# Optimization experiments

Measured on AMD Instinct MI355X. Metric: run time of the kernel, lower is better.

Reference implementation:

```python
import jax, jax.numpy as jnp
import numpy as np

HIDDEN = 4096
N_HEADS = 32
N_KV_HEADS = 8
HEAD_DIM = HIDDEN // N_HEADS  # 128
KV_DIM = N_KV_HEADS * HEAD_DIM  # 1024
ROPE_THETA = 10000.0
B, S = 1, 2048


def setup_inputs() -> dict:
    key = jax.random.key(0)
    ks = jax.random.split(key, 5)
    scale = 0.02
    return {
        "positions": jnp.arange(B * S, dtype=jnp.int32).reshape(B, S),
        "hidden_states": jax.random.normal(ks[0], (B, S, HIDDEN), dtype=jnp.float32),
        "Wqkv": jax.random.normal(ks[1], (HIDDEN, HIDDEN + 2 * KV_DIM), dtype=jnp.float32) * scale,
        "bqkv": jax.random.normal(ks[2], (HIDDEN + 2 * KV_DIM,), dtype=jnp.float32) * scale,
        "Wproj": jax.random.normal(ks[3], (HIDDEN, HIDDEN), dtype=jnp.float32) * scale,
        "bproj": jax.random.normal(ks[4], (HIDDEN,), dtype=jnp.float32) * scale,
    }


def _apply_rope(x, positions):
    # x: [B, S, H, D]; NeoX-style rotation over full head_dim (vLLM get_rope default)
    half = HEAD_DIM // 2
    inv_freq = 1.0 / (ROPE_THETA ** (jnp.arange(0, half, dtype=jnp.float32) / half))
    angles = positions.astype(jnp.float32)[..., None] * inv_freq  # [B, S, half]
    cos = jnp.cos(angles)[:, :, None, :]  # [B, S, 1, half]
    sin = jnp.sin(angles)[:, :, None, :]
    x1, x2 = x[..., :half], x[..., half:]
    return jnp.concatenate([x1 * cos - x2 * sin, x2 * cos + x1 * sin], axis=-1)


def reference(positions, hidden_states, Wqkv, bqkv, Wproj, bproj):
    b, s, _ = hidden_states.shape
    qkv = hidden_states @ Wqkv + bqkv  # [B, S, HIDDEN + 2*KV_DIM]
    q, k, v = jnp.split(qkv, [HIDDEN, HIDDEN + KV_DIM], axis=-1)
    q = q.reshape(b, s, N_HEADS, HEAD_DIM)
    k = k.reshape(b, s, N_KV_HEADS, HEAD_DIM)
    v = v.reshape(b, s, N_KV_HEADS, HEAD_DIM)

    q = _apply_rope(q, positions)
    k = _apply_rope(k, positions)

    # GQA: expand kv heads to query heads (4 query heads per kv head)
    rep = N_HEADS // N_KV_HEADS
    k = jnp.repeat(k, rep, axis=2)  # [B, S, N_HEADS, D]
    v = jnp.repeat(v, rep, axis=2)

    scaling = 1.0 / np.sqrt(HEAD_DIM).astype(np.float32)
    scores = jnp.einsum("bqhd,bkhd->bhqk", q, k) * scaling  # [B, H, S, S]
    causal = jnp.tril(jnp.ones((s, s), dtype=bool))
    scores = jnp.where(causal[None, None], scores, jnp.finfo(scores.dtype).min)
    probs = jax.nn.softmax(scores, axis=-1)
    attn = jnp.einsum("bhqk,bkhd->bqhd", probs, v).reshape(b, s, HIDDEN)

    return attn @ Wproj + bproj
```

## Files before the change

### kernel.cpp

```cpp
#include <hip/hip_runtime.h>

#define HIDDEN 4096
#define NHEADS 32
#define NKV 8
#define HD 128
#define KVD 1024
#define QKVN 6144
#define SEQ 2048

typedef unsigned short u16;
typedef __bf16 bf16x8 __attribute__((ext_vector_type(8)));
typedef float f32x4 __attribute__((ext_vector_type(4)));
typedef unsigned short u16x4 __attribute__((ext_vector_type(4)));

__device__ __forceinline__ u16 f2b(float f) {
  union { float f; unsigned u; } v; v.f = f;
  unsigned r = (v.u + 0x7fffu + ((v.u >> 16) & 1u)) >> 16;
  return (u16)r;
}

__device__ __forceinline__ float b2f(u16 b) {
  union { unsigned u; float f; } v; v.u = ((unsigned)b) << 16;
  return v.f;
}

__device__ __forceinline__ void gl_lds16(const void* g, void* l) {
  __builtin_amdgcn_global_load_lds(
      (const __attribute__((address_space(1))) unsigned*)g,
      (__attribute__((address_space(3))) unsigned*)l, 16, 0, 0);
}

__device__ __forceinline__ f32x4 mfma16(bf16x8 a, bf16x8 b, f32x4 c) {
  return __builtin_amdgcn_mfma_f32_16x16x32_bf16(a, b, c, 0, 0, 0);
}

__global__ void cvt_bf16(const float* __restrict__ x, u16* __restrict__ y, int n) {
  int i = (blockIdx.x * 256 + threadIdx.x) * 4;
  if (i < n) {
    float4 v = *(const float4*)(x + i);
    u16x4 o = {f2b(v.x), f2b(v.y), f2b(v.z), f2b(v.w)};
    *(u16x4*)(y + i) = o;
  }
}

__global__ void transpose_cvt64(const float* __restrict__ W, long ldW,
                                u16* __restrict__ Wt, long ldT) {
  __shared__ float tile[64][65];
  long c0 = blockIdx.x * 64L, r0 = blockIdx.y * 64L;
  int tx = threadIdx.x, ty = threadIdx.y;
#pragma unroll
  for (int i = 0; i < 4; ++i) {
    float4 v = *(const float4*)(W + (r0 + ty + i * 16) * ldW + c0 + tx * 4);
    tile[ty + i * 16][tx * 4 + 0] = v.x;
    tile[ty + i * 16][tx * 4 + 1] = v.y;
    tile[ty + i * 16][tx * 4 + 2] = v.z;
    tile[ty + i * 16][tx * 4 + 3] = v.w;
  }
  __syncthreads();
#pragma unroll
  for (int i = 0; i < 4; ++i) {
    int c = ty + i * 16;
    u16x4 o = {f2b(tile[tx * 4 + 0][c]), f2b(tile[tx * 4 + 1][c]),
               f2b(tile[tx * 4 + 2][c]), f2b(tile[tx * 4 + 3][c])};
    *(u16x4*)(Wt + (c0 + c) * ldT + r0 + tx * 4) = o;
  }
}

__global__ void transpose_b16(const u16* __restrict__ W, long ldW,
                              u16* __restrict__ Wt, long ldT) {
  __shared__ float tile[64][65];
  long c0 = blockIdx.x * 64L, r0 = blockIdx.y * 64L;
  int tx = threadIdx.x, ty = threadIdx.y;
#pragma unroll
  for (int i = 0; i < 4; ++i) {
    u16x4 v = *(const u16x4*)(W + (r0 + ty + i * 16) * ldW + c0 + tx * 4);
    tile[ty + i * 16][tx * 4 + 0] = b2f(v.x);
    tile[ty + i * 16][tx * 4 + 1] = b2f(v.y);
    tile[ty + i * 16][tx * 4 + 2] = b2f(v.z);
    tile[ty + i * 16][tx * 4 + 3] = b2f(v.w);
  }
  __syncthreads();
#pragma unroll
  for (int i = 0; i < 4; ++i) {
    int c = ty + i * 16;
    u16x4 o = {f2b(tile[tx * 4 + 0][c]), f2b(tile[tx * 4 + 1][c]),
               f2b(tile[tx * 4 + 2][c]), f2b(tile[tx * 4 + 3][c])};
    *(u16x4*)(Wt + (c0 + c) * ldT + r0 + tx * 4) = o;
  }
}

__global__ __launch_bounds__(256) void gemm_bt_bias(
    const u16* __restrict__ A, const u16* __restrict__ Bt,
    const float* __restrict__ bias, float* __restrict__ C,
    int M, int N, int K) {
  __shared__ u16 As[128 * 32];
  __shared__ u16 Bs[128 * 32];
  const int t = threadIdx.x;
  const int w = t >> 6, lane = t & 63, quad = lane >> 4, l15 = lane & 15;
  const int wy = w >> 1, wx = w & 1;
  const long m0 = blockIdx.y * 128L, n0 = blockIdx.x * 128L;
  f32x4 acc[4][4] = {};
  const u16* Ag = A + (m0 + (t >> 2)) * (long)K + (t & 3) * 8;
  const u16* Bg = Bt + (n0 + (t >> 2)) * (long)K + (t & 3) * 8;
  char* lA0 = (char*)As + w * 1024;
  char* lA1 = (char*)As + 4096 + w * 1024;
  char* lB0 = (char*)Bs + w * 1024;
  char* lB1 = (char*)Bs + 4096 + w * 1024;
  const long k64 = 64L * K;
  for (int k0 = 0; k0 < K; k0 += 32) {
    gl_lds16(Ag + k0, lA0);
    gl_lds16(Ag + k64 + k0, lA1);
    gl_lds16(Bg + k0, lB0);
    gl_lds16(Bg + k64 + k0, lB1);
    __syncthreads();
    bf16x8 af[4], bfr[4];
#pragma unroll
    for (int mi = 0; mi < 4; ++mi)
      af[mi] = *reinterpret_cast<const bf16x8*>(&As[(wy * 64 + mi * 16 + l15) * 32 + quad * 8]);
#pragma unroll
    for (int nj = 0; nj < 4; ++nj)
      bfr[nj] = *reinterpret_cast<const bf16x8*>(&Bs[(wx * 64 + nj * 16 + l15) * 32 + quad * 8]);
#pragma unroll
    for (int mi = 0; mi < 4; ++mi)
#pragma unroll
      for (int nj = 0; nj < 4; ++nj)
        acc[mi][nj] = mfma16(af[mi], bfr[nj], acc[mi][nj]);
    __syncthreads();
  }
#pragma unroll
  for (int mi = 0; mi < 4; ++mi) {
#pragma unroll
    for (int nj = 0; nj < 4; ++nj) {
      long n = n0 + wx * 64 + nj * 16 + l15;
      float bv = bias[n];
      long mrow = m0 + wy * 64 + mi * 16 + quad * 4;
#pragma unroll
      for (int r = 0; r < 4; ++r)
        C[(mrow + r) * (long)N + n] = acc[mi][nj][r] + bv;
    }
  }
}

__global__ __launch_bounds__(256) void gemm_bt_bias_b16(
    const u16* __restrict__ A, const u16* __restrict__ Bt,
    const float* __restrict__ bias, u16* __restrict__ C,
    int M, int N, int K) {
  __shared__ u16 As[128 * 32];
  __shared__ u16 Bs[128 * 32];
  const int t = threadIdx.x;
  const int w = t >> 6, lane = t & 63, quad = lane >> 4, l15 = lane & 15;
  const int wy = w >> 1, wx = w & 1;
  const long m0 = blockIdx.y * 128L, n0 = blockIdx.x * 128L;
  f32x4 acc[4][4] = {};
  const u16* Ag = A + (m0 + (t >> 2)) * (long)K + (t & 3) * 8;
  const u16* Bg = Bt + (n0 + (t >> 2)) * (long)K + (t & 3) * 8;
  char* lA0 = (char*)As + w * 1024;
  char* lA1 = (char*)As + 4096 + w * 1024;
  char* lB0 = (char*)Bs + w * 1024;
  char* lB1 = (char*)Bs + 4096 + w * 1024;
  const long k64 = 64L * K;
  for (int k0 = 0; k0 < K; k0 += 32) {
    gl_lds16(Ag + k0, lA0);
    gl_lds16(Ag + k64 + k0, lA1);
    gl_lds16(Bg + k0, lB0);
    gl_lds16(Bg + k64 + k0, lB1);
    __syncthreads();
    bf16x8 af[4], bfr[4];
#pragma unroll
    for (int mi = 0; mi < 4; ++mi)
      af[mi] = *reinterpret_cast<const bf16x8*>(&As[(wy * 64 + mi * 16 + l15) * 32 + quad * 8]);
#pragma unroll
    for (int nj = 0; nj < 4; ++nj)
      bfr[nj] = *reinterpret_cast<const bf16x8*>(&Bs[(wx * 64 + nj * 16 + l15) * 32 + quad * 8]);
#pragma unroll
    for (int mi = 0; mi < 4; ++mi)
#pragma unroll
      for (int nj = 0; nj < 4; ++nj)
        acc[mi][nj] = mfma16(af[mi], bfr[nj], acc[mi][nj]);
    __syncthreads();
  }
#pragma unroll
  for (int mi = 0; mi < 4; ++mi) {
#pragma unroll
    for (int nj = 0; nj < 4; ++nj) {
      long n = n0 + wx * 64 + nj * 16 + l15;
      float bv = bias[n];
      long mrow = m0 + wy * 64 + mi * 16 + quad * 4;
#pragma unroll
      for (int r = 0; r < 4; ++r)
        C[(mrow + r) * (long)N + n] = f2b(acc[mi][nj][r] + bv);
    }
  }
}

__global__ void rope_qk(const u16* __restrict__ qkv, const int* __restrict__ pos,
                        u16* __restrict__ Qr, u16* __restrict__ Kr) {
  int s = blockIdx.x;
  int hl = threadIdx.x >> 6;
  int d = threadIdx.x & 63;
  int h = blockIdx.y * 4 + hl;
  float p = (float)pos[s];
  float inv = __builtin_amdgcn_exp2f(-(float)d * (13.287712379549449f / 64.0f));
  float ang = p * inv;
  float cs, sn;
  __sincosf(ang, &sn, &cs);
  long base = (long)s * QKVN + (long)h * HD;
  float x1 = b2f(qkv[base + d]), x2 = b2f(qkv[base + d + 64]);
  float o1 = x1 * cs - x2 * sn, o2 = x2 * cs + x1 * sn;
  if (h < NHEADS) {
    const float sc = 0.12751744154f;
    long ob = ((long)h * SEQ + s) * HD;
    Qr[ob + d] = f2b(o1 * sc);
    Qr[ob + d + 64] = f2b(o2 * sc);
  } else {
    long ob = ((long)(h - NHEADS) * SEQ + s) * HD;
    Kr[ob + d] = f2b(o1);
    Kr[ob + d + 64] = f2b(o2);
  }
}

__device__ __forceinline__ void attn_tile(
    const bf16x8 q[4], const u16* KsF, const u16* VsF, u16* Psw,
    bool diag, int wq, int quad, int l15, int sq, f32x4 Oa[8], f32x4& lacc,
    bf16x8 ones) {
  f32x4 s[4] = {};
#pragma unroll
  for (int ks = 0; ks < 4; ++ks) {
#pragma unroll
    for (int nj = 0; nj < 4; ++nj) {
      bf16x8 bk = *reinterpret_cast<const bf16x8*>(
          &KsF[ks * 2048 + (nj * 16 + l15) * 32 + sq * 8]);
      s[nj] = mfma16(q[ks], bk, s[nj]);
    }
  }
#pragma unroll
  for (int nj = 0; nj < 4; ++nj) {
    int key = nj * 16 + l15;
    int ksw = key >> 5, kc = key & 31;
    int khi = kc >> 3, klo = kc & 7;
#pragma unroll
    for (int r = 0; r < 4; ++r) {
      float x = s[nj][r];
      if (diag && key > wq + r) x = -3.0e30f;
      int row = quad * 4 + r;
      Psw[ksw * 512 + row * 32 + ((khi ^ ((row >> 1) & 3)) << 3) + klo] =
          f2b(__builtin_amdgcn_exp2f(x));
    }
  }
#pragma unroll
  for (int ks = 0; ks < 2; ++ks) {
    bf16x8 ap = *reinterpret_cast<const bf16x8*>(&Psw[ks * 512 + l15 * 32 + sq * 8]);
    lacc = mfma16(ap, ones, lacc);
#pragma unroll
    for (int dj = 0; dj < 8; ++dj) {
      bf16x8 bv = *reinterpret_cast<const bf16x8*>(
          &VsF[ks * 4096 + (dj * 16 + l15) * 32 + sq * 8]);
      Oa[dj] = mfma16(ap, bv, Oa[dj]);
    }
  }
}

__global__ __launch_bounds__(256) void attn_fused(
    const u16* __restrict__ Qr, const u16* __restrict__ Kr,
    const u16* __restrict__ Vt, u16* __restrict__ Ao) {
  __shared__ u16 Ks[4 * 64 * 32];
  __shared__ u16 Vs[2 * 128 * 32];
  __shared__ u16 Ps[4][2 * 16 * 32];
  const int px = blockIdx.x, h = blockIdx.y, kvh = h >> 2;
  const int qtA = px, qtB = (SEQ / 64 - 1) - px;
  const int t = threadIdx.x, w = t >> 6, lane = t & 63;
  const int quad = lane >> 4, l15 = lane & 15;
  const int sq = quad ^ ((l15 >> 1) & 3);
  const int wq = w * 16 + quad * 4;
  u16* Psw = &Ps[w][0];

  bf16x8 ones;
  {
    union { u16 u[8]; bf16x8 v; } ou;
#pragma unroll
    for (int i = 0; i < 8; ++i) ou.u[i] = 0x3F80;
    ones = ou.v;
  }

  const long go = (long)(w * 16 + (lane >> 2)) * HD +
                  (long)(((lane & 3) ^ ((lane >> 3) & 3)) * 8);

  bf16x8 qA[4], qB[4];
  {
    const u16* QgA = Qr + ((long)h * SEQ + qtA * 64) * HD;
    const u16* QgB = Qr + ((long)h * SEQ + qtB * 64) * HD;
#pragma unroll
    for (int j = 0; j < 4; ++j) {
      gl_lds16(QgA + go + j * 32, (char*)Ks + j * 4096 + w * 1024);
      gl_lds16(QgB + go + j * 32, (char*)Vs + j * 4096 + w * 1024);
    }
    __syncthreads();
#pragma unroll
    for (int j = 0; j < 4; ++j) {
      qA[j] = *reinterpret_cast<const bf16x8*>(&Ks[j * 2048 + (w * 16 + l15) * 32 + sq * 8]);
      qB[j] = *reinterpret_cast<const bf16x8*>(&Vs[j * 2048 + (w * 16 + l15) * 32 + sq * 8]);
    }
    __syncthreads();
  }

  f32x4 OaA[8] = {}, OaB[8] = {};
  f32x4 lA = {}, lB = {};
  const u16* Kg0 = Kr + (long)kvh * SEQ * HD;
  const u16* Vg0 = Vt + (long)kvh * HD * SEQ;

  for (int kt = 0; kt <= qtB; ++kt) {
    const int k0 = kt * 64;
    {
      const u16* Kg = Kg0 + (long)k0 * HD;
#pragma unroll
      for (int j = 0; j < 4; ++j)
        gl_lds16(Kg + go + j * 32, (char*)Ks + j * 4096 + w * 1024);
      const u16* Vg = Vg0 + k0;
      const int vc = ((lane & 3) ^ ((lane >> 3) & 3)) * 8;
#pragma unroll
      for (int j = 0; j < 4; ++j) {
        int dd = (j & 1) * 64 + w * 16 + (lane >> 2);
        int ks = j >> 1;
        gl_lds16(Vg + (long)dd * SEQ + ks * 32 + vc, (char*)Vs + j * 4096 + w * 1024);
      }
    }
    __syncthreads();

    attn_tile(qB, Ks, Vs, Psw, kt == qtB, wq, quad, l15, sq, OaB, lB, ones);
    if (kt <= qtA)
      attn_tile(qA, Ks, Vs, Psw, kt == qtA, wq, quad, l15, sq, OaA, lA, ones);

    __syncthreads();
  }

#pragma unroll
  for (int r = 0; r < 4; ++r) {
    float invA = 1.0f / lA[r];
    float invB = 1.0f / lB[r];
    long rowA = (long)(qtA * 64 + w * 16 + quad * 4 + r) * HIDDEN + (long)h * HD;
    long rowB = (long)(qtB * 64 + w * 16 + quad * 4 + r) * HIDDEN + (long)h * HD;
#pragma unroll
    for (int dj = 0; dj < 8; ++dj) {
      Ao[rowA + dj * 16 + l15] = f2b(OaA[dj][r] * invA);
      Ao[rowB + dj * 16 + l15] = f2b(OaB[dj][r] * invB);
    }
  }
}

extern "C" void kernel_launch(void* const* d_in, const int* in_sizes, int n_in,
                              void* d_out, int out_size, void* d_ws, size_t ws_size,
                              hipStream_t stream) {
  const int* positions = (const int*)d_in[0];
  const float* hidden = (const float*)d_in[1];
  const float* Wqkv = (const float*)d_in[2];
  const float* bqkv = (const float*)d_in[3];
  const float* Wproj = (const float*)d_in[4];
  const float* bproj = (const float*)d_in[5];
  float* out = (float*)d_out;
  char* ws = (char*)d_ws;

  u16* Wqt = (u16*)(ws);
  u16* Wpt = (u16*)(ws + 50331648L);
  u16* Xb = (u16*)(ws + 83886080L);
  u16* QKVb = (u16*)(ws + 100663296L);
  u16* Qr = (u16*)(ws + 125829120L);
  u16* Kr = (u16*)(ws + 142606336L);
  u16* Vt = (u16*)(ws + 146800640L);
  u16* Ao = (u16*)(ws + 150994944L);

  cvt_bf16<<<8192, 256, 0, stream>>>(hidden, Xb, SEQ * HIDDEN);
  transpose_cvt64<<<dim3(QKVN / 64, HIDDEN / 64), dim3(16, 16), 0, stream>>>(Wqkv, QKVN, Wqt, HIDDEN);
  transpose_cvt64<<<dim3(HIDDEN / 64, HIDDEN / 64), dim3(16, 16), 0, stream>>>(Wproj, HIDDEN, Wpt, HIDDEN);
  gemm_bt_bias_b16<<<dim3(QKVN / 128, SEQ / 128), 256, 0, stream>>>(Xb, Wqt, bqkv, QKVb, SEQ, QKVN, HIDDEN);
  rope_qk<<<dim3(SEQ, 10), 256, 0, stream>>>(QKVb, positions, Qr, Kr);
  transpose_b16<<<dim3(KVD / 64, SEQ / 64), dim3(16, 16), 0, stream>>>(QKVb + 5120, QKVN, Vt, SEQ);
  attn_fused<<<dim3(SEQ / 128, NHEADS), 256, 0, stream>>>(Qr, Kr, Vt, Ao);
  gemm_bt_bias<<<dim3(HIDDEN / 128, SEQ / 128), 256, 0, stream>>>(Ao, Wpt, bproj, out, SEQ, HIDDEN, HIDDEN);
}
```

Before: 574.6 us.

## Replace GEMMs with 256x256 double-buffered, swizzled-LDS, pipelined MFMA kernel

```diff
diff --git a/kernel.cpp b/kernel.cpp
--- a/kernel.cpp
+++ b/kernel.cpp
@@ -34,6 +34,11 @@
   return __builtin_amdgcn_mfma_f32_16x16x32_bf16(a, b, c, 0, 0, 0);
 }
 
+#define BARRIER() __builtin_amdgcn_s_barrier()
+#define WAIT_LGKM0() asm volatile("s_waitcnt lgkmcnt(0)" ::: "memory")
+#define WAIT_VM6() asm volatile("s_waitcnt vmcnt(6)" ::: "memory")
+#define WAIT_VM0() asm volatile("s_waitcnt vmcnt(0)" ::: "memory")
+
 __global__ void cvt_bf16(const float* __restrict__ x, u16* __restrict__ y, int n) {
   int i = (blockIdx.x * 256 + threadIdx.x) * 4;
   if (i < n) {
@@ -89,106 +94,148 @@
   }
 }
 
-__global__ __launch_bounds__(256) void gemm_bt_bias(
+
+#define LOAD_AF(lA, QM)                                                   \
+  _Pragma("unroll") for (int mi_ = 0; mi_ < 4; ++mi_) {                   \
+    const int ro_ = (wm * 128 + (QM) * 64 + mi_ * 16 + l15) * 64;         \
+    af[mi_][0] = *(const bf16x8*)&(lA)[ro_ + sq0];                        \
+    af[mi_][1] = *(const bf16x8*)&(lA)[ro_ + sq1];                        \
+  }
+
+#define LOAD_BF(lB, QN, DST)                                              \
+  _Pragma("unroll") for (int nj_ = 0; nj_ < 2; ++nj_) {                   \
+    const int ro_ = (wn * 64 + (QN) * 32 + nj_ * 16 + l15) * 64;          \
+    DST[nj_][0] = *(const bf16x8*)&(lB)[ro_ + sq0];                       \
+    DST[nj_][1] = *(const bf16x8*)&(lB)[ro_ + sq1];                       \
+  }
+
+#define MFMA_BLOCK(MI0, NJ0, BFARR)                                       \
+  __builtin_amdgcn_s_setprio(1);                                          \
+  _Pragma("unroll") for (int mi_ = 0; mi_ < 4; ++mi_)                     \
+  _Pragma("unroll") for (int nj_ = 0; nj_ < 2; ++nj_)                     \
+  _Pragma("unroll") for (int ks_ = 0; ks_ < 2; ++ks_)                     \
+    acc[(MI0) + mi_][(NJ0) + nj_] =                                       \
+        mfma16(af[mi_][ks_], BFARR[nj_][ks_], acc[(MI0) + mi_][(NJ0) + nj_]); \
+  __builtin_amdgcn_s_setprio(0);
+
+#define STAGE_A(buf, u, kt)                                               \
+  { char* d_ = dA[u] + (buf) * 32768;                                     \
+    gl_lds16(aS[u][0] + (long)(kt) * 64, d_);                             \
+    gl_lds16(aS[u][1] + (long)(kt) * 64, d_ + 1024); }
+
+#define STAGE_B(buf, u, kt)                                               \
+  { char* d_ = dB[u] + (buf) * 32768;                                     \
+    gl_lds16(bS[u][0] + (long)(kt) * 64, d_);                             \
+    gl_lds16(bS[u][1] + (long)(kt) * 64, d_ + 1024); }
+
+template <bool OUT16>
+__global__ __launch_bounds__(512) void gemm256_bt_bias(
     const u16* __restrict__ A, const u16* __restrict__ Bt,
-    const float* __restrict__ bias, float* __restrict__ C,
+    const float* __restrict__ bias, void* __restrict__ Cv,
     int M, int N, int K) {
-  __shared__ u16 As[128 * 32];
-  __shared__ u16 Bs[128 * 32];
+  __shared__ u16 As[2][16384];
+  __shared__ u16 Bs[2][16384];
   const int t = threadIdx.x;
-  const int w = t >> 6, lane = t & 63, quad = lane >> 4, l15 = lane & 15;
-  const int wy = w >> 1, wx = w & 1;
-  const long m0 = blockIdx.y * 128L, n0 = blockIdx.x * 128L;
-  f32x4 acc[4][4] = {};
-  const u16* Ag = A + (m0 + (t >> 2)) * (long)K + (t & 3) * 8;
-  const u16* Bg = Bt + (n0 + (t >> 2)) * (long)K + (t & 3) * 8;
-  char* lA0 = (char*)As + w * 1024;
-  char* lA1 = (char*)As + 4096 + w * 1024;
-  char* lB0 = (char*)Bs + w * 1024;
-  char* lB1 = (char*)Bs + 4096 + w * 1024;
-  const long k64 = 64L * K;
-  for (int k0 = 0; k0 < K; k0 += 32) {
-    gl_lds16(Ag + k0, lA0);
-    gl_lds16(Ag + k64 + k0, lA1);
-    gl_lds16(Bg + k0, lB0);
-    gl_lds16(Bg + k64 + k0, lB1);
-    __syncthreads();
-    bf16x8 af[4], bfr[4];
-#pragma unroll
-    for (int mi = 0; mi < 4; ++mi)
-      af[mi] = *reinterpret_cast<const bf16x8*>(&As[(wy * 64 + mi * 16 + l15) * 32 + quad * 8]);
-#pragma unroll
-    for (int nj = 0; nj < 4; ++nj)
-      bfr[nj] = *reinterpret_cast<const bf16x8*>(&Bs[(wx * 64 + nj * 16 + l15) * 32 + quad * 8]);
-#pragma unroll
-    for (int mi = 0; mi < 4; ++mi)
-#pragma unroll
-      for (int nj = 0; nj < 4; ++nj)
-        acc[mi][nj] = mfma16(af[mi], bfr[nj], acc[mi][nj]);
-    __syncthreads();
-  }
-#pragma unroll
-  for (int mi = 0; mi < 4; ++mi) {
+  const int w = t >> 6, lane = t & 63;
+  const int quad = lane >> 4, l15 = lane & 15;
+  const int wm = w >> 2, wn = w & 3;
+  const long m0 = blockIdx.y * 256L, n0 = blockIdx.x * 256L;
+  const int NT = K >> 6;
+
+  const int sq0 = ((quad ^ (l15 & 7)) << 3);
+  const int sq1 = sq0 ^ 32;
+
+  const int xs8 = ((lane & 7) ^ (lane >> 3)) * 8;
+  const int sr = lane >> 3;
+  const u16 *aS[2][2], *bS[2][2];
+  char *dA[2], *dB[2];
+  {
+    const int ra = (w >> 2) * 128 + (w & 3) * 16;
+    const int rb = w * 16;
+#pragma unroll
+    for (int u = 0; u < 2; ++u) {
+#pragma unroll
+      for (int j = 0; j < 2; ++j) {
+        aS[u][j] = A + (m0 + ra + u * 64 + j * 8 + sr) * (long)K + xs8;
+        bS[u][j] = Bt + (n0 + rb + u * 128 + j * 8 + sr) * (long)K + xs8;
+      }
+    }
+    dA[0] = (char*)As + ra * 128;
+    dA[1] = (char*)As + (ra + 64) * 128;
+    dB[0] = (char*)Bs + rb * 128;
+    dB[1] = (char*)Bs + (rb + 128) * 128;
+  }
+
+  f32x4 acc[8][4] = {};
+  bf16x8 af[4][2], bfA[2][2], bfB[2][2];
+
+  STAGE_A(0, 0, 0); STAGE_A(0, 1, 0); STAGE_B(0, 0, 0); STAGE_B(0, 1, 0);
+  STAGE_A(1, 0, 1); STAGE_B(1, 0, 1); STAGE_B(1, 1, 1);
+  WAIT_VM6();
+  BARRIER();
+
+  for (int T = 0; T < NT; T += 2) {
+    const bool live = (T + 2 < NT);
+    LOAD_AF(As[0], 0);
+    LOAD_BF(Bs[0], 0, bfA);
+    STAGE_A(1, 1, T + 1);
+    BARRIER(); WAIT_LGKM0();
+    MFMA_BLOCK(0, 0, bfA);
+    BARRIER();
+    LOAD_BF(Bs[0], 1, bfB);
+    if (live) STAGE_A(0, 0, T + 2);
+    BARRIER(); WAIT_LGKM0();
+    MFMA_BLOCK(0, 2, bfB);
+    BARRIER();
+    LOAD_AF(As[0], 1);
+    if (live) STAGE_B(0, 0, T + 2);
+    BARRIER(); WAIT_LGKM0();
+    MFMA_BLOCK(4, 2, bfB);
+    BARRIER();
+    if (live) { STAGE_B(0, 1, T + 2); WAIT_VM6(); } else { WAIT_VM0(); }
+    BARRIER();
+    MFMA_BLOCK(4, 0, bfA);
+    BARRIER();
+    LOAD_AF(As[1], 0);
+    LOAD_BF(Bs[1], 0, bfA);
+    if (live) STAGE_A(0, 1, T + 2);
+    BARRIER(); WAIT_LGKM0();
+    MFMA_BLOCK(0, 0, bfA);
+    BARRIER();
+    LOAD_BF(Bs[1], 1, bfB);
+    if (live) STAGE_A(1, 0, T + 3);
+    BARRIER(); WAIT_LGKM0();
+    MFMA_BLOCK(0, 2, bfB);
+    BARRIER();
+    LOAD_AF(As[1], 1);
+    if (live) STAGE_B(1, 0, T + 3);
+    BARRIER(); WAIT_LGKM0();
+    MFMA_BLOCK(4, 2, bfB);
+    BARRIER();
+    if (live) { STAGE_B(1, 1, T + 3); WAIT_VM6(); } else { WAIT_VM0(); }
+    BARRIER();
+    MFMA_BLOCK(4, 0, bfA);
+    BARRIER();
+  }
+
+#pragma unroll
+  for (int mi = 0; mi < 8; ++mi) {
 #pragma unroll
     for (int nj = 0; nj < 4; ++nj) {
-      long n = n0 + wx * 64 + nj * 16 + l15;
+      long n = n0 + wn * 64 + nj * 16 + l15;
       float bv = bias[n];
-      long mrow = m0 + wy * 64 + mi * 16 + quad * 4;
-#pragma unroll
-      for (int r = 0; r < 4; ++r)
-        C[(mrow + r) * (long)N + n] = acc[mi][nj][r] + bv;
-    }
-  }
-}
-
-__global__ __launch_bounds__(256) void gemm_bt_bias_b16(
-    const u16* __restrict__ A, const u16* __restrict__ Bt,
-    const float* __restrict__ bias, u16* __restrict__ C,
-    int M, int N, int K) {
-  __shared__ u16 As[128 * 32];
-  __shared__ u16 Bs[128 * 32];
-  const int t = threadIdx.x;
-  const int w = t >> 6, lane = t & 63, quad = lane >> 4, l15 = lane & 15;
-  const int wy = w >> 1, wx = w & 1;
-  const long m0 = blockIdx.y * 128L, n0 = blockIdx.x * 128L;
-  f32x4 acc[4][4] = {};
-  const u16* Ag = A + (m0 + (t >> 2)) * (long)K + (t & 3) * 8;
-  const u16* Bg = Bt + (n0 + (t >> 2)) * (long)K + (t & 3) * 8;
-  char* lA0 = (char*)As + w * 1024;
-  char* lA1 = (char*)As + 4096 + w * 1024;
-  char* lB0 = (char*)Bs + w * 1024;
-  char* lB1 = (char*)Bs + 4096 + w * 1024;
-  const long k64 = 64L * K;
-  for (int k0 = 0; k0 < K; k0 += 32) {
-    gl_lds16(Ag + k0, lA0);
-    gl_lds16(Ag + k64 + k0, lA1);
-    gl_lds16(Bg + k0, lB0);
-    gl_lds16(Bg + k64 + k0, lB1);
-    __syncthreads();
-    bf16x8 af[4], bfr[4];
-#pragma unroll
-    for (int mi = 0; mi < 4; ++mi)
-      af[mi] = *reinterpret_cast<const bf16x8*>(&As[(wy * 64 + mi * 16 + l15) * 32 + quad * 8]);
-#pragma unroll
-    for (int nj = 0; nj < 4; ++nj)
-      bfr[nj] = *reinterpret_cast<const bf16x8*>(&Bs[(wx * 64 + nj * 16 + l15) * 32 + quad * 8]);
-#pragma unroll
-    for (int mi = 0; mi < 4; ++mi)
-#pragma unroll
-      for (int nj = 0; nj < 4; ++nj)
-        acc[mi][nj] = mfma16(af[mi], bfr[nj], acc[mi][nj]);
-    __syncthreads();
-  }
-#pragma unroll
-  for (int mi = 0; mi < 4; ++mi) {
-#pragma unroll
-    for (int nj = 0; nj < 4; ++nj) {
-      long n = n0 + wx * 64 + nj * 16 + l15;
-      float bv = bias[n];
-      long mrow = m0 + wy * 64 + mi * 16 + quad * 4;
-#pragma unroll
-      for (int r = 0; r < 4; ++r)
-        C[(mrow + r) * (long)N + n] = f2b(acc[mi][nj][r] + bv);
+      long mr = m0 + wm * 128 + mi * 16 + quad * 4;
+      if constexpr (OUT16) {
+        u16* C = (u16*)Cv;
+#pragma unroll
+        for (int r = 0; r < 4; ++r)
+          C[(mr + r) * (long)N + n] = f2b(acc[mi][nj][r] + bv);
+      } else {
+        float* C = (float*)Cv;
+#pragma unroll
+        for (int r = 0; r < 4; ++r)
+          C[(mr + r) * (long)N + n] = acc[mi][nj][r] + bv;
+      }
     }
   }
 }
@@ -371,9 +418,9 @@
   cvt_bf16<<<8192, 256, 0, stream>>>(hidden, Xb, SEQ * HIDDEN);
   transpose_cvt64<<<dim3(QKVN / 64, HIDDEN / 64), dim3(16, 16), 0, stream>>>(Wqkv, QKVN, Wqt, HIDDEN);
   transpose_cvt64<<<dim3(HIDDEN / 64, HIDDEN / 64), dim3(16, 16), 0, stream>>>(Wproj, HIDDEN, Wpt, HIDDEN);
-  gemm_bt_bias_b16<<<dim3(QKVN / 128, SEQ / 128), 256, 0, stream>>>(Xb, Wqt, bqkv, QKVb, SEQ, QKVN, HIDDEN);
+  gemm256_bt_bias<true><<<dim3(QKVN / 256, SEQ / 256), 512, 0, stream>>>(Xb, Wqt, bqkv, QKVb, SEQ, QKVN, HIDDEN);
   rope_qk<<<dim3(SEQ, 10), 256, 0, stream>>>(QKVb, positions, Qr, Kr);
   transpose_b16<<<dim3(KVD / 64, SEQ / 64), dim3(16, 16), 0, stream>>>(QKVb + 5120, QKVN, Vt, SEQ);
   attn_fused<<<dim3(SEQ / 128, NHEADS), 256, 0, stream>>>(Qr, Kr, Vt, Ao);
-  gemm_bt_bias<<<dim3(HIDDEN / 128, SEQ / 128), 256, 0, stream>>>(Ao, Wpt, bproj, out, SEQ, HIDDEN, HIDDEN);
-}
+  gemm256_bt_bias<false><<<dim3(HIDDEN / 256, SEQ / 256), 512, 0, stream>>>(Ao, Wpt, bproj, out, SEQ, HIDDEN, HIDDEN);
+}
```

Result: no change. 583.3 us (+1.5%).
